# Optimization experiments

Hardware: AMD Instinct MI355X
Metric: run time of the kernel (lower is better)

Reference implementation:

```python
import jax, jax.numpy as jnp
import numpy as np

NUM_HEADS = 8


def setup_inputs() -> dict:
    key = jax.random.key(0)
    ks = jax.random.split(key, 8)
    B, N, H, W = 8, 1024, 32, 32
    dim = H * W  # 1024
    x1 = jax.random.normal(ks[0], (B, N, H, W), dtype=jnp.float32)
    x2 = jax.random.normal(ks[1], (B, N, H, W), dtype=jnp.float32)
    conv_w = jax.random.normal(ks[2], (N, 2 * N, 3, 3), dtype=jnp.float32) * 0.01
    conv_b = jnp.zeros((N,), dtype=jnp.float32)
    wq = jax.random.normal(ks[3], (dim, dim), dtype=jnp.float32) * 0.02
    wk = jax.random.normal(ks[4], (dim, dim), dtype=jnp.float32) * 0.02
    wv = jax.random.normal(ks[5], (dim, dim), dtype=jnp.float32) * 0.02
    proj_w = jax.random.normal(ks[6], (dim, dim), dtype=jnp.float32) * 0.02
    proj_b = jnp.zeros((dim,), dtype=jnp.float32)
    return {"x1": x1, "x2": x2, "conv_w": conv_w, "conv_b": conv_b,
            "wq": wq, "wk": wk, "wv": wv, "proj_w": proj_w, "proj_b": proj_b}


def reference(x1, x2, conv_w, conv_b, wq, wk, wv, proj_w, proj_b):
    B, N, H, W = x1.shape
    C = H * W
    nh = NUM_HEADS
    hd = C // nh
    scale = hd ** -0.5

    # conv_cat: Conv2d(2N -> N, k=3, pad=1) on channel-concatenated inputs
    x_cat = jnp.concatenate([x1, x2], axis=1)  # [B, 2N, H, W]
    x_cat = jax.lax.conv_general_dilated(
        x_cat, conv_w, window_strides=(1, 1), padding=((1, 1), (1, 1)),
        dimension_numbers=("NCHW", "OIHW", "NCHW"))
    x_cat = x_cat + conv_b[None, :, None, None]
    x_cat = x_cat.reshape(B, N, C)  # [B, N, C]

    # torch Linear: y = x @ W.T (no bias, qkv_bias=False)
    def heads(t):  # [B, N, C] -> [B, nh, N, hd]
        return t.reshape(B, N, nh, hd).transpose(0, 2, 1, 3)

    q = heads(x1.reshape(B, N, C) @ wq.T)
    k = heads(x_cat @ wk.T)
    v = heads(x_cat @ wv.T)

    # attention: softmax(q k^T * scale) v   (dropout is identity at p=0)
    attn = jnp.einsum("bhnd,bhmd->bhnm", q, k) * scale
    attn = jax.nn.softmax(attn, axis=-1)
    x_attn = jnp.einsum("bhnm,bhmd->bhnd", attn, v)  # [B, nh, N, hd]
    x_attn = x_attn.transpose(0, 2, 1, 3).reshape(B, N, C)

    out = (x_attn @ proj_w.T + proj_b).reshape(B, N, H, W) + x1
    return out
```

## Files before the change

kernel.cpp:

```cpp
#include <hip/hip_runtime.h>
#include <hip/hip_bf16.h>
#include <cstdint>
#include <cstddef>

typedef __attribute__((ext_vector_type(8))) short short8;
typedef __attribute__((ext_vector_type(4))) float f32x4;
typedef unsigned short u16;

static __device__ __forceinline__ u16 f2bf(float f) {
  __hip_bfloat16 h = __float2bfloat16(f);
  return *reinterpret_cast<u16*>(&h);
}

static __device__ __forceinline__ void gload16(const void* g, void* l) {
  __builtin_amdgcn_global_load_lds(
      (const __attribute__((address_space(1))) void*)g,
      (__attribute__((address_space(3))) void*)l, 16, 0, 0);
}


__global__ void cast_k(const float* __restrict__ in, u16* __restrict__ out, int n4) {
  int i = blockIdx.x * 256 + threadIdx.x;
  if (i < n4) {
    float4 v = ((const float4*)in)[i];
    union { u16 u[4]; uint2 p; } r;
    r.u[0] = f2bf(v.x); r.u[1] = f2bf(v.y); r.u[2] = f2bf(v.z); r.u[3] = f2bf(v.w);
    ((uint2*)out)[i] = r.p;
  }
}

__global__ void build_int(const float* __restrict__ x1, const float* __restrict__ x2,
                          u16* __restrict__ in_t) {
  __shared__ float tile[64][65];
  const int it = blockIdx.x;
  const int st = blockIdx.y;
  const int b  = blockIdx.z;
  const int i0 = it * 64, s0 = st * 64;
  const float* src = (i0 < 1024)
      ? x1 + ((size_t)b * 1024 + i0) * 1024
      : x2 + ((size_t)b * 1024 + (i0 - 1024)) * 1024;
  const int t = threadIdx.x;
  #pragma unroll
  for (int jj = 0; jj < 16; ++jj) {
    int idx = jj * 256 + t;
    int ii = idx >> 6, si = idx & 63;
    tile[ii][si] = src[(size_t)ii * 1024 + s0 + si];
  }
  __syncthreads();
  #pragma unroll
  for (int jj = 0; jj < 16; ++jj) {
    int idx = jj * 256 + t;
    int si = idx >> 6, ii = idx & 63;
    in_t[((size_t)b * 1024 + s0 + si) * 2048 + i0 + ii] = f2bf(tile[ii][si]);
  }
}

__global__ void pack_wp(const float* __restrict__ cw, u16* __restrict__ Wp) {
  __shared__ float sb[2304];
  const int blk = blockIdx.x;
  const int t = threadIdx.x;
  const size_t base = (size_t)blk * 2304;
  #pragma unroll
  for (int jj = 0; jj < 9; ++jj) sb[jj * 256 + t] = cw[base + jj * 256 + t];
  __syncthreads();
  const int p = blk * 256 + t;
  #pragma unroll
  for (int q = 0; q < 9; ++q)
    Wp[(size_t)q * 2097152 + p] = f2bf(sb[t * 9 + q]);
}

__global__ void zero_k(u16* z) { z[threadIdx.x] = 0; }


enum { GM_PLAIN = 0, GM_VT = 1, GM_PROJ = 2, GM_CONV = 3, GM_KV = 4 };

template<int MODE>
__global__ __launch_bounds__(512, 2)
void gemm4_k(const u16* __restrict__ A, const u16* __restrict__ B,
             u16* __restrict__ Cb, u16* __restrict__ Cb2, float* __restrict__ Cf,
             const float* __restrict__ bias, const float* __restrict__ resid,
             const u16* __restrict__ zb, int Ktot, int ntn_sh) {
  __shared__ u16 lds[3 * 24576];
  const int tid = threadIdx.x;
  const int lane = tid & 63;
  const int w = tid >> 6;
  const int l15 = lane & 15, l4 = lane >> 4;

  const int nwg = gridDim.x;
  const int bid = blockIdx.x;
  const int lb = (bid & 7) * (nwg >> 3) + (bid >> 3);
  const int tm = lb >> ntn_sh;
  const int tn = lb & ((1 << ntn_sh) - 1);
  const int row0 = tm * 256, col0 = tn * 128;
  const int wr = (w >> 1) * 64, wc = (w & 1) * 64;

  const int sr = w * 8 + (lane >> 3);
  const int pp = (lane & 7) ^ (lane >> 3);

  int am[4], ay[4], ax[4];
  #pragma unroll
  for (int u = 0; u < 4; ++u) {
    const int m = row0 + u * 64 + sr;
    am[u] = m;
    const int s = m & 1023;
    ay[u] = s >> 5; ax[u] = s & 31;
  }

  f32x4 acc[4][4];
  #pragma unroll
  for (int i = 0; i < 4; ++i)
    #pragma unroll
    for (int jj = 0; jj < 4; ++jj)
      acc[i][jj] = (f32x4){0.f, 0.f, 0.f, 0.f};

  const int nK = Ktot >> 6;

  auto stageA = [&](int kt, u16* buf) {
    u16* da = buf + (size_t)w * 512;
    if constexpr (MODE == GM_CONV) {
      const int q = kt >> 5;
      const int ks0 = (kt & 31) << 6;
      const int qd = (q >= 6) ? 2 : (q >= 3) ? 1 : 0;
      const int dy = qd - 1, dx = q - qd * 3 - 1;
      const int dd = (dy << 5) + dx;
      #pragma unroll
      for (int u = 0; u < 3; ++u) {
        const int yy = ay[u] + dy, xx = ax[u] + dx;
        const bool valid = ((unsigned)yy < 32u) && ((unsigned)xx < 32u);
        const u16* ga = valid ? A + (((size_t)(am[u] + dd)) << 11) + ks0 + pp * 8 : zb;
        gload16(ga, da + u * 4096);
      }
    } else {
      const int k0 = kt << 6;
      #pragma unroll
      for (int u = 0; u < 3; ++u) {
        const u16* ga = A + (size_t)(row0 + u * 64 + sr) * Ktot + k0 + pp * 8;
        gload16(ga, da + u * 4096);
      }
    }
  };
  auto stageB = [&](int kt, u16* buf) {
    u16* da = buf + (size_t)w * 512;
    u16* db = buf + 16384 + (size_t)w * 512;
    if constexpr (MODE == GM_CONV) {
      const int q = kt >> 5;
      const int ks0 = (kt & 31) << 6;
      const int qd = (q >= 6) ? 2 : (q >= 3) ? 1 : 0;
      const int dy = qd - 1, dx = q - qd * 3 - 1;
      const int dd = (dy << 5) + dx;
      {
        const int yy = ay[3] + dy, xx = ax[3] + dx;
        const bool valid = ((unsigned)yy < 32u) && ((unsigned)xx < 32u);
        const u16* ga = valid ? A + (((size_t)(am[3] + dd)) << 11) + ks0 + pp * 8 : zb;
        gload16(ga, da + 3 * 4096);
      }
      const size_t boff = ((size_t)q << 21) + ks0 + pp * 8;
      #pragma unroll
      for (int u = 0; u < 2; ++u) {
        const u16* gb = B + boff + ((size_t)(col0 + u * 64 + sr) << 11);
        gload16(gb, db + u * 4096);
      }
    } else {
      const int k0 = kt << 6;
      {
        const u16* ga = A + (size_t)(row0 + 3 * 64 + sr) * Ktot + k0 + pp * 8;
        gload16(ga, da + 3 * 4096);
      }
      #pragma unroll
      for (int u = 0; u < 2; ++u) {
        const u16* gb = B + (size_t)(col0 + u * 64 + sr) * Ktot + k0 + pp * 8;
        gload16(gb, db + u * 4096);
      }
    }
  };

  u16* pb0 = lds;
  u16* pb1 = lds + 24576;
  u16* pb2 = lds + 49152;

  stageA(0, pb0); stageB(0, pb0);
  stageA(1, pb1); stageB(1, pb1);
  asm volatile("s_waitcnt vmcnt(6)" ::: "memory");
  __builtin_amdgcn_s_barrier();

  for (int t = 0; t < nK; ++t) {
    const char* Ar = (const char*)pb0;
    const char* Br = (const char*)(pb0 + 16384);
    {
      const int bcol = (l4 << 4) ^ ((l15 & 7) << 4);
      short8 av[4], bv[4];
      #pragma unroll
      for (int mi = 0; mi < 4; ++mi)
        av[mi] = *(const short8*)(Ar + (wr + mi * 16 + l15) * 128 + bcol);
      #pragma unroll
      for (int ni = 0; ni < 4; ++ni)
        bv[ni] = *(const short8*)(Br + (wc + ni * 16 + l15) * 128 + bcol);
      if (t + 2 < nK) stageA(t + 2, pb2);
      __builtin_amdgcn_s_barrier();
      asm volatile("s_waitcnt lgkmcnt(0)" ::: "memory");
      __builtin_amdgcn_sched_barrier(0);
      __builtin_amdgcn_s_setprio(1);
      #pragma unroll
      for (int mi = 0; mi < 4; ++mi)
        #pragma unroll
        for (int ni = 0; ni < 4; ++ni)
          acc[mi][ni] = __builtin_amdgcn_mfma_f32_16x16x32_bf16(av[mi], bv[ni], acc[mi][ni], 0, 0, 0);
      __builtin_amdgcn_s_setprio(0);
      __builtin_amdgcn_s_barrier();
    }
    {
      const int bcol = (64 + (l4 << 4)) ^ ((l15 & 7) << 4);
      short8 av[4], bv[4];
      #pragma unroll
      for (int mi = 0; mi < 4; ++mi)
        av[mi] = *(const short8*)(Ar + (wr + mi * 16 + l15) * 128 + bcol);
      #pragma unroll
      for (int ni = 0; ni < 4; ++ni)
        bv[ni] = *(const short8*)(Br + (wc + ni * 16 + l15) * 128 + bcol);
      if (t + 2 < nK) {
        stageB(t + 2, pb2);
        asm volatile("s_waitcnt vmcnt(6)" ::: "memory");
      } else if (t + 1 < nK) {
        asm volatile("s_waitcnt vmcnt(0)" ::: "memory");
      }
      __builtin_amdgcn_s_barrier();
      asm volatile("s_waitcnt lgkmcnt(0)" ::: "memory");
      __builtin_amdgcn_sched_barrier(0);
      __builtin_amdgcn_s_setprio(1);
      #pragma unroll
      for (int mi = 0; mi < 4; ++mi)
        #pragma unroll
        for (int ni = 0; ni < 4; ++ni)
          acc[mi][ni] = __builtin_amdgcn_mfma_f32_16x16x32_bf16(av[mi], bv[ni], acc[mi][ni], 0, 0, 0);
      __builtin_amdgcn_s_setprio(0);
      __builtin_amdgcn_s_barrier();
    }
    u16* tmp = pb0; pb0 = pb1; pb1 = pb2; pb2 = tmp;
  }

  #pragma unroll
  for (int mi = 0; mi < 4; ++mi) {
    #pragma unroll
    for (int ni = 0; ni < 4; ++ni) {
      #pragma unroll
      for (int j = 0; j < 4; ++j) {
        const int grow = row0 + wr + mi * 16 + l4 * 4 + j;
        const int gcol = col0 + wc + ni * 16 + l15;
        const float v = acc[mi][ni][j];
        if constexpr (MODE == GM_PLAIN) {
          Cb[((size_t)grow << 10) + gcol] = f2bf(v);
        } else if constexpr (MODE == GM_VT) {
          const int b = grow >> 10, ms = grow & 1023;
          const int h = gcol >> 7, d = gcol & 127;
          Cb[((size_t)((b * 8 + h) * 128 + d) << 10) + ms] = f2bf(v);
        } else if constexpr (MODE == GM_KV) {
          if (gcol < 1024) {
            Cb[((size_t)grow << 10) + gcol] = f2bf(v);
          } else {
            const int c = gcol - 1024;
            const int b = grow >> 10, ms = grow & 1023;
            const int h = c >> 7, d = c & 127;
            Cb2[((size_t)((b * 8 + h) * 128 + d) << 10) + ms] = f2bf(v);
          }
        } else if constexpr (MODE == GM_PROJ) {
          const size_t o = ((size_t)grow << 10) + gcol;
          Cf[o] = v + bias[gcol] + resid[o];
        } else {
          const int b = grow >> 10, s = grow & 1023;
          Cb[((size_t)((b << 10) + gcol) << 10) + s] = f2bf(v + bias[gcol]);
        }
      }
    }
  }
}

__global__ __launch_bounds__(256, 2)
void attn2_k(const u16* __restrict__ Q, const u16* __restrict__ K,
             const u16* __restrict__ Vt, u16* __restrict__ O) {
  __shared__ u16 Ks[2][64 * 128];
  __shared__ u16 Vs[2][128 * 64];
  __shared__ u16 Plds[4][16 * 80];
  const int mtile = blockIdx.x;
  const int bh = blockIdx.y;
  const int b = bh >> 3, h = bh & 7;
  const int tid = threadIdx.x, lane = tid & 63, w = tid >> 6;
  const int l15 = lane & 15, l4 = lane >> 4;

  short8 qf[4];
  {
    const int qrow = b * 1024 + mtile * 64 + w * 16 + l15;
    const u16* qb = Q + ((size_t)qrow << 10) + h * 128;
    #pragma unroll
    for (int kk = 0; kk < 4; ++kk)
      qf[kk] = *(const short8*)(qb + kk * 32 + l4 * 8);
  }

  f32x4 o[8];
  #pragma unroll
  for (int db = 0; db < 8; ++db) o[db] = (f32x4){0.f, 0.f, 0.f, 0.f};
  float mrow[4], lrow[4];
  #pragma unroll
  for (int j = 0; j < 4; ++j) { mrow[j] = -1e30f; lrow[j] = 0.f; }
  const float scale = 0.08838834764831845f;

  auto stageKV = [&](int kt, int half) {
    #pragma unroll
    for (int j = 0; j < 4; ++j) {
      const int c = (j * 4 + w) * 64 + lane;
      const int r = c >> 4;
      const int coff = (((c & 15) ^ (r & 7)) << 3);
      const u16* gp = K + ((size_t)(b * 1024 + kt * 64 + r) << 10) + h * 128 + coff;
      gload16(gp, (void*)(Ks[half] + (j * 4 + w) * 512));
    }
    #pragma unroll
    for (int j = 0; j < 4; ++j) {
      const int c = (j * 4 + w) * 64 + lane;
      const int r = c >> 3;
      const int coff = (((c & 7) ^ (r & 7)) << 3);
      const u16* gp = Vt + ((size_t)((b * 8 + h) * 128 + r) << 10) + kt * 64 + coff;
      gload16(gp, (void*)(Vs[half] + (j * 4 + w) * 512));
    }
  };

  stageKV(0, 0);
  for (int kt = 0; kt < 16; ++kt) {
    const int cur = kt & 1;
    asm volatile("s_waitcnt vmcnt(0)" ::: "memory");
    __builtin_amdgcn_s_barrier();
    if (kt + 1 < 16) stageKV(kt + 1, cur ^ 1);

    const u16* ks_ = Ks[cur];
    const u16* vs_ = Vs[cur];
    f32x4 s[4];
    #pragma unroll
    for (int cb = 0; cb < 4; ++cb) {
      s[cb] = (f32x4){0.f, 0.f, 0.f, 0.f};
      #pragma unroll
      for (int kk = 0; kk < 4; ++kk) {
        const int col = (kk * 32 + l4 * 8) ^ ((l15 & 7) << 3);
        short8 bK = *(const short8*)(ks_ + (cb * 16 + l15) * 128 + col);
        s[cb] = __builtin_amdgcn_mfma_f32_16x16x32_bf16(qf[kk], bK, s[cb], 0, 0, 0);
      }
    }
    #pragma unroll
    for (int cb = 0; cb < 4; ++cb) {
      s[cb][0] *= scale; s[cb][1] *= scale; s[cb][2] *= scale; s[cb][3] *= scale;
    }
    #pragma unroll
    for (int j = 0; j < 4; ++j) {
      float mx = fmaxf(fmaxf(s[0][j], s[1][j]), fmaxf(s[2][j], s[3][j]));
      #pragma unroll
      for (int off = 8; off >= 1; off >>= 1)
        mx = fmaxf(mx, __shfl_xor(mx, off, 64));
      const float mn = fmaxf(mrow[j], mx);
      const float fac = __expf(mrow[j] - mn);
      mrow[j] = mn;
      float rs = 0.f;
      #pragma unroll
      for (int cb = 0; cb < 4; ++cb) {
        const float p = __expf(s[cb][j] - mn);
        s[cb][j] = p;
        rs += p;
      }
      #pragma unroll
      for (int off = 8; off >= 1; off >>= 1)
        rs += __shfl_xor(rs, off, 64);
      lrow[j] = lrow[j] * fac + rs;
      #pragma unroll
      for (int db = 0; db < 8; ++db) o[db][j] *= fac;
    }
    u16* pl = Plds[w];
    #pragma unroll
    for (int cb = 0; cb < 4; ++cb)
      #pragma unroll
      for (int j = 0; j < 4; ++j)
        pl[(l4 * 4 + j) * 80 + cb * 16 + l15] = f2bf(s[cb][j]);
    asm volatile("s_waitcnt lgkmcnt(0)" ::: "memory");
    __builtin_amdgcn_sched_barrier(0);
    short8 ap[2];
    #pragma unroll
    for (int ks2 = 0; ks2 < 2; ++ks2)
      ap[ks2] = *(const short8*)(pl + l15 * 80 + ks2 * 32 + l4 * 8);
    #pragma unroll
    for (int db = 0; db < 8; ++db) {
      #pragma unroll
      for (int ks2 = 0; ks2 < 2; ++ks2) {
        const int col = (ks2 * 32 + l4 * 8) ^ ((l15 & 7) << 3);
        short8 bV = *(const short8*)(vs_ + (db * 16 + l15) * 64 + col);
        o[db] = __builtin_amdgcn_mfma_f32_16x16x32_bf16(ap[ks2], bV, o[db], 0, 0, 0);
      }
    }
  }
  #pragma unroll
  for (int db = 0; db < 8; ++db) {
    #pragma unroll
    for (int j = 0; j < 4; ++j) {
      const int grow = b * 1024 + mtile * 64 + w * 16 + l4 * 4 + j;
      const int gcol = h * 128 + db * 16 + l15;
      O[((size_t)grow << 10) + gcol] = f2bf(o[db][j] / lrow[j]);
    }
  }
}


extern "C" void kernel_launch(void* const* d_in, const int* in_sizes, int n_in,
                              void* d_out, int out_size, void* d_ws, size_t ws_size,
                              hipStream_t stream) {
  const float* x1     = (const float*)d_in[0];
  const float* x2     = (const float*)d_in[1];
  const float* conv_w = (const float*)d_in[2];
  const float* conv_b = (const float*)d_in[3];
  const float* wq     = (const float*)d_in[4];
  const float* wk     = (const float*)d_in[5];
  const float* wv     = (const float*)d_in[6];
  const float* proj_w = (const float*)d_in[7];
  const float* proj_b = (const float*)d_in[8];
  float* out = (float*)d_out;

  char* ws = (char*)d_ws;
  size_t off = 0;
  auto alloc = [&](size_t bytes) -> void* {
    void* p = ws + off;
    off += (bytes + 255) & ~(size_t)255;
    return p;
  };
  u16* x1b  = (u16*)alloc(8192ULL * 1024 * 2);
  u16* in_t = (u16*)alloc(8ULL * 1024 * 2048 * 2);
  u16* Wp   = (u16*)alloc(9ULL * 2097152 * 2);
  u16* wqb  = (u16*)alloc(1048576ULL * 2);
  u16* wkb  = (u16*)alloc(1048576ULL * 2);
  u16* wvb  = (u16*)alloc(1048576ULL * 2);
  u16* pjb  = (u16*)alloc(1048576ULL * 2);
  u16* xc   = (u16*)alloc(8192ULL * 1024 * 2);
  u16* Qb   = (u16*)alloc(8192ULL * 1024 * 2);
  u16* Kb   = (u16*)alloc(8192ULL * 1024 * 2);
  u16* Vtb  = (u16*)alloc(8192ULL * 1024 * 2);
  u16* Ob   = (u16*)alloc(8192ULL * 1024 * 2);
  u16* zb   = (u16*)alloc(256);

  cast_k<<<8192, 256, 0, stream>>>(x1, x1b, 2097152);
  cast_k<<<1024, 256, 0, stream>>>(wq, wqb, 262144);
  cast_k<<<1024, 256, 0, stream>>>(wk, wkb, 262144);
  cast_k<<<1024, 256, 0, stream>>>(wv, wvb, 262144);
  cast_k<<<1024, 256, 0, stream>>>(proj_w, pjb, 262144);
  build_int<<<dim3(32, 16, 8), 256, 0, stream>>>(x1, x2, in_t);
  pack_wp<<<8192, 256, 0, stream>>>(conv_w, Wp);
  zero_k<<<1, 128, 0, stream>>>(zb);

  gemm4_k<GM_CONV><<<256, 512, 0, stream>>>(in_t, Wp, xc, nullptr, nullptr, conv_b, nullptr, zb, 18432, 3);
  gemm4_k<GM_PLAIN><<<256, 512, 0, stream>>>(x1b, wqb, Qb, nullptr, nullptr, nullptr, nullptr, zb, 1024, 3);
  gemm4_k<GM_KV><<<512, 512, 0, stream>>>(xc, wkb, Kb, Vtb, nullptr, nullptr, nullptr, zb, 1024, 4);
  attn2_k<<<dim3(16, 64), 256, 0, stream>>>(Qb, Kb, Vtb, Ob);
  gemm4_k<GM_PROJ><<<256, 512, 0, stream>>>(Ob, pjb, nullptr, nullptr, out, proj_b, x1, zb, 1024, 3);
}
```

Baseline: 604.3 us.

## Split-K conv GEMM with smaller K-tiles, fuse cast kernels, simplify GEMM pipeline

```diff
diff --git a/kernel.cpp b/kernel.cpp
--- a/kernel.cpp
+++ b/kernel.cpp
@@ -19,24 +19,29 @@
 }
 
 
-__global__ void cast_k(const float* __restrict__ in, u16* __restrict__ out, int n4) {
+__global__ void cast4_k(const float* __restrict__ a, const float* __restrict__ b,
+                        const float* __restrict__ c, const float* __restrict__ d,
+                        u16* __restrict__ oa, u16* __restrict__ ob,
+                        u16* __restrict__ oc, u16* __restrict__ od) {
+  const int which = blockIdx.y;
+  const float* src = (which == 0) ? a : (which == 1) ? b : (which == 2) ? c : d;
+  u16* dst = (which == 0) ? oa : (which == 1) ? ob : (which == 2) ? oc : od;
   int i = blockIdx.x * 256 + threadIdx.x;
-  if (i < n4) {
-    float4 v = ((const float4*)in)[i];
-    union { u16 u[4]; uint2 p; } r;
-    r.u[0] = f2bf(v.x); r.u[1] = f2bf(v.y); r.u[2] = f2bf(v.z); r.u[3] = f2bf(v.w);
-    ((uint2*)out)[i] = r.p;
-  }
-}
-
-__global__ void build_int(const float* __restrict__ x1, const float* __restrict__ x2,
-                          u16* __restrict__ in_t) {
+  float4 v = ((const float4*)src)[i];
+  union { u16 u[4]; uint2 p; } r;
+  r.u[0] = f2bf(v.x); r.u[1] = f2bf(v.y); r.u[2] = f2bf(v.z); r.u[3] = f2bf(v.w);
+  ((uint2*)dst)[i] = r.p;
+}
+
+__global__ void build_int2(const float* __restrict__ x1, const float* __restrict__ x2,
+                           u16* __restrict__ in_t, u16* __restrict__ x1b) {
   __shared__ float tile[64][65];
   const int it = blockIdx.x;
   const int st = blockIdx.y;
   const int b  = blockIdx.z;
   const int i0 = it * 64, s0 = st * 64;
-  const float* src = (i0 < 1024)
+  const bool isx1 = (i0 < 1024);
+  const float* src = isx1
       ? x1 + ((size_t)b * 1024 + i0) * 1024
       : x2 + ((size_t)b * 1024 + (i0 - 1024)) * 1024;
   const int t = threadIdx.x;
@@ -44,7 +49,10 @@
   for (int jj = 0; jj < 16; ++jj) {
     int idx = jj * 256 + t;
     int ii = idx >> 6, si = idx & 63;
-    tile[ii][si] = src[(size_t)ii * 1024 + s0 + si];
+    float v = src[(size_t)ii * 1024 + s0 + si];
+    tile[ii][si] = v;
+    if (isx1)
+      x1b[((size_t)b * 1024 + i0 + ii) * 1024 + s0 + si] = f2bf(v);
   }
   __syncthreads();
   #pragma unroll
@@ -71,15 +79,39 @@
 
 __global__ void zero_k(u16* z) { z[threadIdx.x] = 0; }
 
+__global__ void addc_k(const float* __restrict__ p, const float* __restrict__ bias,
+                       u16* __restrict__ xc) {
+  __shared__ float tile[64][65];
+  const int st = blockIdx.x;
+  const int ot = blockIdx.y;
+  const int b  = blockIdx.z;
+  const int s0 = st * 64, o0 = ot * 64;
+  const int t = threadIdx.x;
+  const float* p1 = p + 8388608;
+  #pragma unroll
+  for (int jj = 0; jj < 16; ++jj) {
+    int idx = jj * 256 + t;
+    int si = idx >> 6, oi = idx & 63;
+    const size_t m = ((size_t)b * 1024 + s0 + si) * 1024 + o0 + oi;
+    tile[si][oi] = p[m] + p1[m] + bias[o0 + oi];
+  }
+  __syncthreads();
+  #pragma unroll
+  for (int jj = 0; jj < 16; ++jj) {
+    int idx = jj * 256 + t;
+    int oi = idx >> 6, si = idx & 63;
+    xc[((size_t)b * 1024 + o0 + oi) * 1024 + s0 + si] = f2bf(tile[si][oi]);
+  }
+}
 
 enum { GM_PLAIN = 0, GM_VT = 1, GM_PROJ = 2, GM_CONV = 3, GM_KV = 4 };
 
 template<int MODE>
 __global__ __launch_bounds__(512, 2)
-void gemm4_k(const u16* __restrict__ A, const u16* __restrict__ B,
-             u16* __restrict__ Cb, u16* __restrict__ Cb2, float* __restrict__ Cf,
+void gemm3_k(const u16* __restrict__ A, const u16* __restrict__ B,
+             u16* __restrict__ Cb, float* __restrict__ Cf,
              const float* __restrict__ bias, const float* __restrict__ resid,
-             const u16* __restrict__ zb, int Ktot, int ntn_sh) {
+             int Ktot, int ntn_sh) {
   __shared__ u16 lds[3 * 24576];
   const int tid = threadIdx.x;
   const int lane = tid & 63;
@@ -97,15 +129,6 @@
   const int sr = w * 8 + (lane >> 3);
   const int pp = (lane & 7) ^ (lane >> 3);
 
-  int am[4], ay[4], ax[4];
-  #pragma unroll
-  for (int u = 0; u < 4; ++u) {
-    const int m = row0 + u * 64 + sr;
-    am[u] = m;
-    const int s = m & 1023;
-    ay[u] = s >> 5; ax[u] = s & 31;
-  }
-
   f32x4 acc[4][4];
   #pragma unroll
   for (int i = 0; i < 4; ++i)
@@ -115,79 +138,28 @@
 
   const int nK = Ktot >> 6;
 
-  auto stageA = [&](int kt, u16* buf) {
-    u16* da = buf + (size_t)w * 512;
-    if constexpr (MODE == GM_CONV) {
-      const int q = kt >> 5;
-      const int ks0 = (kt & 31) << 6;
-      const int qd = (q >= 6) ? 2 : (q >= 3) ? 1 : 0;
-      const int dy = qd - 1, dx = q - qd * 3 - 1;
-      const int dd = (dy << 5) + dx;
-      #pragma unroll
-      for (int u = 0; u < 3; ++u) {
-        const int yy = ay[u] + dy, xx = ax[u] + dx;
-        const bool valid = ((unsigned)yy < 32u) && ((unsigned)xx < 32u);
-        const u16* ga = valid ? A + (((size_t)(am[u] + dd)) << 11) + ks0 + pp * 8 : zb;
-        gload16(ga, da + u * 4096);
-      }
-    } else {
-      const int k0 = kt << 6;
-      #pragma unroll
-      for (int u = 0; u < 3; ++u) {
-        const u16* ga = A + (size_t)(row0 + u * 64 + sr) * Ktot + k0 + pp * 8;
-        gload16(ga, da + u * 4096);
-      }
-    }
-  };
-  auto stageB = [&](int kt, u16* buf) {
+  auto stage = [&](int kt, u16* buf) {
     u16* da = buf + (size_t)w * 512;
     u16* db = buf + 16384 + (size_t)w * 512;
-    if constexpr (MODE == GM_CONV) {
-      const int q = kt >> 5;
-      const int ks0 = (kt & 31) << 6;
-      const int qd = (q >= 6) ? 2 : (q >= 3) ? 1 : 0;
-      const int dy = qd - 1, dx = q - qd * 3 - 1;
-      const int dd = (dy << 5) + dx;
-      {
-        const int yy = ay[3] + dy, xx = ax[3] + dx;
-        const bool valid = ((unsigned)yy < 32u) && ((unsigned)xx < 32u);
-        const u16* ga = valid ? A + (((size_t)(am[3] + dd)) << 11) + ks0 + pp * 8 : zb;
-        gload16(ga, da + 3 * 4096);
-      }
-      const size_t boff = ((size_t)q << 21) + ks0 + pp * 8;
-      #pragma unroll
-      for (int u = 0; u < 2; ++u) {
-        const u16* gb = B + boff + ((size_t)(col0 + u * 64 + sr) << 11);
-        gload16(gb, db + u * 4096);
-      }
-    } else {
-      const int k0 = kt << 6;
-      {
-        const u16* ga = A + (size_t)(row0 + 3 * 64 + sr) * Ktot + k0 + pp * 8;
-        gload16(ga, da + 3 * 4096);
-      }
-      #pragma unroll
-      for (int u = 0; u < 2; ++u) {
-        const u16* gb = B + (size_t)(col0 + u * 64 + sr) * Ktot + k0 + pp * 8;
-        gload16(gb, db + u * 4096);
-      }
+    const int k0 = kt << 6;
+    #pragma unroll
+    for (int u = 0; u < 4; ++u) {
+      const u16* ga = A + (size_t)(row0 + u * 64 + sr) * Ktot + k0 + pp * 8;
+      gload16(ga, da + u * 4096);
+    }
+    #pragma unroll
+    for (int u = 0; u < 2; ++u) {
+      const u16* gb = B + (size_t)(col0 + u * 64 + sr) * Ktot + k0 + pp * 8;
+      gload16(gb, db + u * 4096);
     }
   };
 
-  u16* pb0 = lds;
-  u16* pb1 = lds + 24576;
-  u16* pb2 = lds + 49152;
-
-  stageA(0, pb0); stageB(0, pb0);
-  stageA(1, pb1); stageB(1, pb1);
-  asm volatile("s_waitcnt vmcnt(6)" ::: "memory");
-  __builtin_amdgcn_s_barrier();
-
-  for (int t = 0; t < nK; ++t) {
-    const char* Ar = (const char*)pb0;
-    const char* Br = (const char*)(pb0 + 16384);
-    {
-      const int bcol = (l4 << 4) ^ ((l15 & 7) << 4);
+  auto compute = [&](const u16* buf) {
+    const char* Ar = (const char*)buf;
+    const char* Br = (const char*)(buf + 16384);
+    #pragma unroll
+    for (int ks = 0; ks < 2; ++ks) {
+      const int bcol = ((ks << 6) + (l4 << 4)) ^ ((l15 & 7) << 4);
       short8 av[4], bv[4];
       #pragma unroll
       for (int mi = 0; mi < 4; ++mi)
@@ -195,10 +167,6 @@
       #pragma unroll
       for (int ni = 0; ni < 4; ++ni)
         bv[ni] = *(const short8*)(Br + (wc + ni * 16 + l15) * 128 + bcol);
-      if (t + 2 < nK) stageA(t + 2, pb2);
-      __builtin_amdgcn_s_barrier();
-      asm volatile("s_waitcnt lgkmcnt(0)" ::: "memory");
-      __builtin_amdgcn_sched_barrier(0);
       __builtin_amdgcn_s_setprio(1);
       #pragma unroll
       for (int mi = 0; mi < 4; ++mi)
@@ -206,35 +174,24 @@
         for (int ni = 0; ni < 4; ++ni)
           acc[mi][ni] = __builtin_amdgcn_mfma_f32_16x16x32_bf16(av[mi], bv[ni], acc[mi][ni], 0, 0, 0);
       __builtin_amdgcn_s_setprio(0);
-      __builtin_amdgcn_s_barrier();
-    }
-    {
-      const int bcol = (64 + (l4 << 4)) ^ ((l15 & 7) << 4);
-      short8 av[4], bv[4];
-      #pragma unroll
-      for (int mi = 0; mi < 4; ++mi)
-        av[mi] = *(const short8*)(Ar + (wr + mi * 16 + l15) * 128 + bcol);
-      #pragma unroll
-      for (int ni = 0; ni < 4; ++ni)
-        bv[ni] = *(const short8*)(Br + (wc + ni * 16 + l15) * 128 + bcol);
-      if (t + 2 < nK) {
-        stageB(t + 2, pb2);
-        asm volatile("s_waitcnt vmcnt(6)" ::: "memory");
-      } else if (t + 1 < nK) {
-        asm volatile("s_waitcnt vmcnt(0)" ::: "memory");
-      }
-      __builtin_amdgcn_s_barrier();
-      asm volatile("s_waitcnt lgkmcnt(0)" ::: "memory");
-      __builtin_amdgcn_sched_barrier(0);
-      __builtin_amdgcn_s_setprio(1);
-      #pragma unroll
-      for (int mi = 0; mi < 4; ++mi)
-        #pragma unroll
-        for (int ni = 0; ni < 4; ++ni)
-          acc[mi][ni] = __builtin_amdgcn_mfma_f32_16x16x32_bf16(av[mi], bv[ni], acc[mi][ni], 0, 0, 0);
-      __builtin_amdgcn_s_setprio(0);
-      __builtin_amdgcn_s_barrier();
-    }
+    }
+  };
+
+  u16* pb0 = lds;
+  u16* pb1 = lds + 24576;
+  u16* pb2 = lds + 49152;
+
+  stage(0, pb0);
+  stage(1, pb1);
+  for (int t = 0; t < nK; ++t) {
+    if (t + 1 < nK) {
+      asm volatile("s_waitcnt vmcnt(6)" ::: "memory");
+    } else {
+      asm volatile("s_waitcnt vmcnt(0)" ::: "memory");
+    }
+    __builtin_amdgcn_s_barrier();
+    if (t + 2 < nK) stage(t + 2, pb2);
+    compute(pb0);
     u16* tmp = pb0; pb0 = pb1; pb1 = pb2; pb2 = tmp;
   }
 
@@ -249,10 +206,149 @@
         const float v = acc[mi][ni][j];
         if constexpr (MODE == GM_PLAIN) {
           Cb[((size_t)grow << 10) + gcol] = f2bf(v);
-        } else if constexpr (MODE == GM_VT) {
-          const int b = grow >> 10, ms = grow & 1023;
-          const int h = gcol >> 7, d = gcol & 127;
-          Cb[((size_t)((b * 8 + h) * 128 + d) << 10) + ms] = f2bf(v);
+        } else if constexpr (MODE == GM_PROJ) {
+          const size_t o = ((size_t)grow << 10) + gcol;
+          Cf[o] = v + bias[gcol] + resid[o];
+        }
+      }
+    }
+  }
+}
+
+template<int MODE, int SPLITK>
+__global__ __launch_bounds__(512, 4)
+void gemm5_k(const u16* __restrict__ A, const u16* __restrict__ B,
+             u16* __restrict__ Cb, u16* __restrict__ Cb2, float* __restrict__ Cf,
+             const u16* __restrict__ zb, int Ktot, int ntn_sh) {
+  __shared__ u16 lds[3 * 12288];
+  const int tid = threadIdx.x;
+  const int lane = tid & 63;
+  const int w = tid >> 6;
+  const int l15 = lane & 15, l4 = lane >> 4;
+
+  const int nwg = gridDim.x;
+  const int bid = blockIdx.x;
+  const int lb = (bid & 7) * (nwg >> 3) + (bid >> 3);
+  int kz = 0, lbt = lb;
+  if constexpr (SPLITK) { kz = lb >> 8; lbt = lb & 255; }
+  const int tm = lbt >> ntn_sh;
+  const int tn = lbt & ((1 << ntn_sh) - 1);
+  const int row0 = tm * 256, col0 = tn * 128;
+  const int wr = (w >> 1) * 64, wc = (w & 1) * 64;
+
+  const int str = tid >> 2;
+  const int sgc = tid & 3;
+
+  int am[2], ay[2], ax[2];
+  #pragma unroll
+  for (int u = 0; u < 2; ++u) {
+    const int m = row0 + u * 128 + str;
+    am[u] = m;
+    const int s = m & 1023;
+    ay[u] = s >> 5; ax[u] = s & 31;
+  }
+
+  f32x4 acc[4][4];
+  #pragma unroll
+  for (int i = 0; i < 4; ++i)
+    #pragma unroll
+    for (int jj = 0; jj < 4; ++jj)
+      acc[i][jj] = (f32x4){0.f, 0.f, 0.f, 0.f};
+
+  const int nKt = Ktot >> 5;
+  const int kbase = SPLITK ? kz * Ktot : 0;
+
+  auto stage = [&](int kt, u16* buf) {
+    const int gk0 = kbase + (kt << 5);
+    if constexpr (MODE == GM_CONV) {
+      const int q = gk0 >> 11;
+      const int ks0 = gk0 & 2047;
+      const int qd = (q >= 6) ? 2 : (q >= 3) ? 1 : 0;
+      const int dy = qd - 1, dx = q - qd * 3 - 1;
+      const int dd = (dy << 5) + dx;
+      #pragma unroll
+      for (int u = 0; u < 2; ++u) {
+        const int r = u * 128 + str;
+        const int swz = sgc ^ ((r >> 1) & 3);
+        const int yy = ay[u] + dy, xx = ax[u] + dx;
+        const bool valid = ((unsigned)yy < 32u) && ((unsigned)xx < 32u);
+        const u16* ga = valid ? A + (((size_t)(am[u] + dd)) << 11) + ks0 + swz * 8 : zb;
+        gload16(ga, buf + ((size_t)u * 512 + tid) * 8);
+      }
+      {
+        const int swz = sgc ^ ((str >> 1) & 3);
+        const u16* gb = B + ((size_t)q << 21) + ((size_t)(col0 + str) << 11) + ks0 + swz * 8;
+        gload16(gb, buf + 8192 + (size_t)tid * 8);
+      }
+    } else {
+      const int k0 = gk0;
+      #pragma unroll
+      for (int u = 0; u < 2; ++u) {
+        const int r = u * 128 + str;
+        const int swz = sgc ^ ((r >> 1) & 3);
+        const u16* ga = A + (size_t)(row0 + r) * Ktot + k0 + swz * 8;
+        gload16(ga, buf + ((size_t)u * 512 + tid) * 8);
+      }
+      {
+        const int swz = sgc ^ ((str >> 1) & 3);
+        const u16* gb = B + (size_t)(col0 + str) * Ktot + k0 + swz * 8;
+        gload16(gb, buf + 8192 + (size_t)tid * 8);
+      }
+    }
+  };
+
+  auto compute = [&](const u16* buf) {
+    short8 av[4], bv[4];
+    #pragma unroll
+    for (int mi = 0; mi < 4; ++mi) {
+      const int row = wr + mi * 16 + l15;
+      const int g = l4 ^ ((row >> 1) & 3);
+      av[mi] = *(const short8*)(buf + row * 32 + g * 8);
+    }
+    #pragma unroll
+    for (int ni = 0; ni < 4; ++ni) {
+      const int row = wc + ni * 16 + l15;
+      const int g = l4 ^ ((row >> 1) & 3);
+      bv[ni] = *(const short8*)(buf + 8192 + row * 32 + g * 8);
+    }
+    __builtin_amdgcn_s_setprio(1);
+    #pragma unroll
+    for (int mi = 0; mi < 4; ++mi)
+      #pragma unroll
+      for (int ni = 0; ni < 4; ++ni)
+        acc[mi][ni] = __builtin_amdgcn_mfma_f32_16x16x32_bf16(av[mi], bv[ni], acc[mi][ni], 0, 0, 0);
+    __builtin_amdgcn_s_setprio(0);
+  };
+
+  u16* pb0 = lds;
+  u16* pb1 = lds + 12288;
+  u16* pb2 = lds + 24576;
+
+  stage(0, pb0);
+  stage(1, pb1);
+  for (int t = 0; t < nKt; ++t) {
+    if (t + 1 < nKt) {
+      asm volatile("s_waitcnt vmcnt(3)" ::: "memory");
+    } else {
+      asm volatile("s_waitcnt vmcnt(0)" ::: "memory");
+    }
+    __builtin_amdgcn_s_barrier();
+    if (t + 2 < nKt) stage(t + 2, pb2);
+    compute(pb0);
+    u16* tmp = pb0; pb0 = pb1; pb1 = pb2; pb2 = tmp;
+  }
+
+  #pragma unroll
+  for (int mi = 0; mi < 4; ++mi) {
+    #pragma unroll
+    for (int ni = 0; ni < 4; ++ni) {
+      #pragma unroll
+      for (int j = 0; j < 4; ++j) {
+        const int grow = row0 + wr + mi * 16 + l4 * 4 + j;
+        const int gcol = col0 + wc + ni * 16 + l15;
+        const float v = acc[mi][ni][j];
+        if constexpr (MODE == GM_CONV) {
+          Cf[(size_t)kz * 8388608 + ((size_t)grow << 10) + gcol] = v;
         } else if constexpr (MODE == GM_KV) {
           if (gcol < 1024) {
             Cb[((size_t)grow << 10) + gcol] = f2bf(v);
@@ -262,12 +358,6 @@
             const int h = c >> 7, d = c & 127;
             Cb2[((size_t)((b * 8 + h) * 128 + d) << 10) + ms] = f2bf(v);
           }
-        } else if constexpr (MODE == GM_PROJ) {
-          const size_t o = ((size_t)grow << 10) + gcol;
-          Cf[o] = v + bias[gcol] + resid[o];
-        } else {
-          const int b = grow >> 10, s = grow & 1023;
-          Cb[((size_t)((b << 10) + gcol) << 10) + s] = f2bf(v + bias[gcol]);
         }
       }
     }
@@ -437,19 +527,17 @@
   u16* Vtb  = (u16*)alloc(8192ULL * 1024 * 2);
   u16* Ob   = (u16*)alloc(8192ULL * 1024 * 2);
   u16* zb   = (u16*)alloc(256);
-
-  cast_k<<<8192, 256, 0, stream>>>(x1, x1b, 2097152);
-  cast_k<<<1024, 256, 0, stream>>>(wq, wqb, 262144);
-  cast_k<<<1024, 256, 0, stream>>>(wk, wkb, 262144);
-  cast_k<<<1024, 256, 0, stream>>>(wv, wvb, 262144);
-  cast_k<<<1024, 256, 0, stream>>>(proj_w, pjb, 262144);
-  build_int<<<dim3(32, 16, 8), 256, 0, stream>>>(x1, x2, in_t);
+  float* pConv = (float*)Qb;
+
+  cast4_k<<<dim3(1024, 4), 256, 0, stream>>>(wq, wk, wv, proj_w, wqb, wkb, wvb, pjb);
+  build_int2<<<dim3(32, 16, 8), 256, 0, stream>>>(x1, x2, in_t, x1b);
   pack_wp<<<8192, 256, 0, stream>>>(conv_w, Wp);
   zero_k<<<1, 128, 0, stream>>>(zb);
 
-  gemm4_k<GM_CONV><<<256, 512, 0, stream>>>(in_t, Wp, xc, nullptr, nullptr, conv_b, nullptr, zb, 18432, 3);
-  gemm4_k<GM_PLAIN><<<256, 512, 0, stream>>>(x1b, wqb, Qb, nullptr, nullptr, nullptr, nullptr, zb, 1024, 3);
-  gemm4_k<GM_KV><<<512, 512, 0, stream>>>(xc, wkb, Kb, Vtb, nullptr, nullptr, nullptr, zb, 1024, 4);
+  gemm5_k<GM_CONV, 1><<<512, 512, 0, stream>>>(in_t, Wp, nullptr, nullptr, pConv, zb, 9216, 3);
+  addc_k<<<dim3(16, 16, 8), 256, 0, stream>>>(pConv, conv_b, xc);
+  gemm3_k<GM_PLAIN><<<256, 512, 0, stream>>>(x1b, wqb, Qb, nullptr, nullptr, nullptr, 1024, 3);
+  gemm5_k<GM_KV, 0><<<512, 512, 0, stream>>>(xc, wkb, Kb, Vtb, nullptr, zb, 1024, 4);
   attn2_k<<<dim3(16, 64), 256, 0, stream>>>(Qb, Kb, Vtb, Ob);
-  gemm4_k<GM_PROJ><<<256, 512, 0, stream>>>(Ob, pjb, nullptr, nullptr, out, proj_b, x1, zb, 1024, 3);
-}
+  gemm3_k<GM_PROJ><<<256, 512, 0, stream>>>(Ob, pjb, nullptr, out, proj_b, x1, 1024, 3);
+}
```

Result: faster. 588.2 us (-2.7%).
